# Kernel tuning notes

Hardware: AMD Instinct MI355X
Metric: run time of the kernel (lower is better)

The kernel has to match this reference:

```python
import jax, jax.numpy as jnp
import numpy as np

N, D = 8192, 256
NUM_CLASSES = 100
WEIGHT = 1.0


def setup_inputs() -> dict:
    key = jax.random.key(0)
    k1, k2 = jax.random.split(key)
    predictions = jax.random.normal(k1, (N, D), dtype=jnp.float32)
    targets = jax.random.randint(k2, (N,), 0, NUM_CLASSES, dtype=jnp.int32)
    return {"predictions": predictions, "targets": targets}


def reference(predictions, targets):
    # Pairwise squared L2 via ||a||^2 + ||b||^2 - 2 a.b  -> [N, N]
    sq = jnp.sum(predictions * predictions, axis=1)
    d2 = sq[:, None] + sq[None, :] - 2.0 * (predictions @ predictions.T)
    dist = jnp.sqrt(jnp.maximum(d2, 0.0))  # torch.dist(p=2)

    n = predictions.shape[0]
    upper = jnp.triu(jnp.ones((n, n), dtype=bool), k=1)  # i < j pairs only
    same = targets[:, None] == targets[None, :]
    mask = upper & same

    num = jnp.sum(mask).astype(dist.dtype)
    loss = jnp.sum(jnp.where(mask, dist, 0.0)) / num
    return loss * WEIGHT
```

## Files before the change

### kernel.cpp

```cpp
#include <hip/hip_runtime.h>

#define N_CLS 100
#define D_DIM 256
#define MAX_M 112
#define ROW_SH 264
#define PANEL 48

typedef short bf16x8 __attribute__((ext_vector_type(8)));
typedef float f32x4  __attribute__((ext_vector_type(4)));

__device__ __forceinline__ unsigned short f2bf(float f) {
    unsigned int b = __float_as_uint(f);
    return (unsigned short)((b + 0x7FFFu + ((b >> 16) & 1u)) >> 16);
}

__device__ __forceinline__ void stage(const float* __restrict__ pred,
        const int* bkt, int m, int cp0, int dslot, int cnt,
        short* tileS, float* sqs, int wave, int lane) {
    for (int r = wave; r < cnt; r += 8) {
        int cp = cp0 + r;
        float4 v = make_float4(0.f, 0.f, 0.f, 0.f);
        if (cp < m) {
            int g = bkt[cp];
            v = ((const float4*)(pred + (size_t)g * D_DIM))[lane];
        }
        short4 pk;
        pk.x = (short)f2bf(v.x); pk.y = (short)f2bf(v.y);
        pk.z = (short)f2bf(v.z); pk.w = (short)f2bf(v.w);
        *(short4*)&tileS[(dslot + r) * ROW_SH + lane * 4] = pk;
        float s = v.x * v.x + v.y * v.y + v.z * v.z + v.w * v.w;
        #pragma unroll
        for (int o = 32; o; o >>= 1) s += __shfl_xor(s, o, 64);
        if (lane == 0) sqs[dslot + r] = s;
    }
}

__device__ __forceinline__ float tile16(const short* tileS, const float* sqs,
        int a0, int b0, int ga0, int gb0, int m, int lane) {
    const int q = lane >> 4, l15 = lane & 15;
    const short* aP = &tileS[(a0 + l15) * ROW_SH + q * 8];
    const short* bP = &tileS[(b0 + l15) * ROW_SH + q * 8];
    f32x4 acc = {0.f, 0.f, 0.f, 0.f};
    #pragma unroll
    for (int ks = 0; ks < 8; ++ks) {
        bf16x8 af = *(const bf16x8*)(aP + ks * 32);
        bf16x8 bg = *(const bf16x8*)(bP + ks * 32);
        acc = __builtin_amdgcn_mfma_f32_16x16x32_bf16(af, bg, acc, 0, 0, 0);
    }
    float out = 0.f;
    #pragma unroll
    for (int rr = 0; rr < 4; ++rr) {
        int al = q * 4 + rr;
        int pi = ga0 + al, pj = gb0 + l15;
        float d2 = sqs[a0 + al] + sqs[b0 + l15] - 2.f * acc[rr];
        if (pj < m && pi < pj) out += sqrtf(fmaxf(d2, 0.f));
    }
    return out;
}

__global__ __launch_bounds__(512) void k_gram(const float* __restrict__ pred,
        const int* __restrict__ targets, int n, int* __restrict__ bucket_g,
        double* __restrict__ psum, double* __restrict__ pcnt, float* __restrict__ out) {
    __shared__ short tileS[MAX_M * ROW_SH];
    __shared__ float sqs[MAX_M];
    __shared__ float wsum[8];
    __shared__ int bkt_s[MAX_M];
    __shared__ int cnt_s;
    const int t = threadIdx.x, lane = t & 63, wave = t >> 6;
    const int c = blockIdx.x;
    int* bkt_g = bucket_g + (size_t)c * n;

    if (t == 0) cnt_s = 0;
    __syncthreads();
    for (int i = t; i < n; i += 512)
        if (targets[i] == c) {
            int pos = atomicAdd(&cnt_s, 1);
            if (pos < MAX_M) bkt_s[pos] = i;
            bkt_g[pos] = i;
        }
    __syncthreads();
    const int m = cnt_s;
    float accum = 0.f;

    if (m <= MAX_M) {
        const int T = (m + 15) >> 4;
        stage(pred, bkt_s, m, 0, 0, T * 16, tileS, sqs, wave, lane);
        __syncthreads();
        const int np = T * (T + 1) / 2;
        for (int idx = wave; idx < np; idx += 8) {
            int ta = 0, r = idx;
            while (r >= T - ta) { r -= T - ta; ++ta; }
            int tb = ta + r;
            accum += tile16(tileS, sqs, ta * 16, tb * 16, ta * 16, tb * 16, m, lane);
        }
    } else {
        const int P = (m + PANEL - 1) / PANEL;
        for (int pi = 0; pi < P; ++pi)
        for (int pj = pi; pj < P; ++pj) {
            __syncthreads();
            stage(pred, bkt_g, m, pi * PANEL, 0,     PANEL, tileS, sqs, wave, lane);
            stage(pred, bkt_g, m, pj * PANEL, PANEL, PANEL, tileS, sqs, wave, lane);
            __syncthreads();
            for (int idx = wave; idx < 9; idx += 8) {
                int ta = idx / 3, tb = idx % 3;
                accum += tile16(tileS, sqs, ta * 16, PANEL + tb * 16,
                                pi * PANEL + ta * 16, pj * PANEL + tb * 16, m, lane);
            }
        }
    }

    #pragma unroll
    for (int o = 32; o; o >>= 1) accum += __shfl_xor(accum, o, 64);
    if (lane == 0) wsum[wave] = accum;
    __syncthreads();
    if (t == 0) {
        double bs = 0.0;
        #pragma unroll
        for (int w = 0; w < 8; ++w) bs += (double)wsum[w];
        __hip_atomic_store(&psum[c], bs, __ATOMIC_RELAXED, __HIP_MEMORY_SCOPE_AGENT);
        __hip_atomic_store(&pcnt[c], (double)m * (double)(m - 1) * 0.5,
                           __ATOMIC_RELEASE, __HIP_MEMORY_SCOPE_AGENT);
    }

    if (c == 0) {
        double mys = 0.0, myc = 0.0;
        if (t < N_CLS) {
            unsigned long long bits;
            do {
                bits = __hip_atomic_load((const unsigned long long*)&pcnt[t],
                                         __ATOMIC_ACQUIRE, __HIP_MEMORY_SCOPE_AGENT);
            } while (bits >> 63);
            myc = __longlong_as_double((long long)bits);
            unsigned long long sb = __hip_atomic_load((const unsigned long long*)&psum[t],
                                         __ATOMIC_RELAXED, __HIP_MEMORY_SCOPE_AGENT);
            mys = __longlong_as_double((long long)sb);
        }
        __syncthreads();
        double* red_s = (double*)tileS;
        double* red_c = red_s + 128;
        if (t < 128) { red_s[t] = (t < N_CLS) ? mys : 0.0;
                       red_c[t] = (t < N_CLS) ? myc : 0.0; }
        __syncthreads();
        for (int w = 64; w; w >>= 1) {
            if (t < w) { red_s[t] += red_s[t + w]; red_c[t] += red_c[t + w]; }
            __syncthreads();
        }
        if (t == 0) out[0] = (float)(red_c[0] > 0.0 ? red_s[0] / red_c[0] : 0.0);
    }
}

extern "C" void kernel_launch(void* const* d_in, const int* in_sizes, int n_in,
                              void* d_out, int out_size, void* d_ws, size_t ws_size,
                              hipStream_t stream) {
    const float* pred  = (const float*)d_in[0];
    const int* targets = (const int*)d_in[1];
    float* out         = (float*)d_out;
    const int n = in_sizes[1];

    char* ws = (char*)d_ws;
    size_t off = 0;
    double* psum     = (double*)(ws + off); off += N_CLS * 8;
    double* pcnt     = (double*)(ws + off); off += N_CLS * 8;
    int*    bucket_g = (int*)(ws + off);

    k_gram<<<N_CLS, 512, 0, stream>>>(pred, targets, n, bucket_g, psum, pcnt, out);
}
```

Before: 74.00 us.

## Split class bucketing and bf16 packing into a separate per-row prep kernel

A new prep kernel assigns one wave per sample row. Each wave atomically appends the row to its class bucket, computes its squared norm and writes a bf16-packed copy into a per-class contiguous buffer. The gram kernel then reads the class count and copies the pre-packed tile straight into shared memory. This replaces the old scheme where each of the 100 blocks scanned all targets and gathered fp32 rows serially. The per-class counters use a poison-value offset and are reset at the end, so correctness depends on the workspace being pre-filled with that pattern; it also adds a second launch.

```diff
diff --git a/kernel.cpp b/kernel.cpp
--- a/kernel.cpp
+++ b/kernel.cpp
@@ -5,6 +5,9 @@
 #define MAX_M 112
 #define ROW_SH 264
 #define PANEL 48
+#define PACK_CAP 128
+#define CNT_STR 32
+#define POISON 0xAAAAAAAAu
 
 typedef short bf16x8 __attribute__((ext_vector_type(8)));
 typedef float f32x4  __attribute__((ext_vector_type(4)));
@@ -12,6 +15,33 @@
 __device__ __forceinline__ unsigned short f2bf(float f) {
     unsigned int b = __float_as_uint(f);
     return (unsigned short)((b + 0x7FFFu + ((b >> 16) & 1u)) >> 16);
+}
+
+__global__ __launch_bounds__(256) void k_prep(const float* __restrict__ pred,
+        const int* __restrict__ targets, int n, int* __restrict__ cnt,
+        int* __restrict__ bucket_g, float* __restrict__ sqp,
+        unsigned short* __restrict__ packed) {
+    const int wid  = (int)((blockIdx.x * 256u + threadIdx.x) >> 6);
+    const int lane = threadIdx.x & 63;
+    if (wid >= n) return;
+    const int c = targets[wid];
+    int pos = 0;
+    if (lane == 0) {
+        pos = (int)((unsigned)atomicAdd(&cnt[c * CNT_STR], 1) - POISON);
+        bucket_g[(size_t)c * n + pos] = wid;
+    }
+    pos = __shfl(pos, 0, 64);
+    const float4 v = ((const float4*)(pred + (size_t)wid * D_DIM))[lane];
+    float s = v.x * v.x + v.y * v.y + v.z * v.z + v.w * v.w;
+    #pragma unroll
+    for (int o = 32; o; o >>= 1) s += __shfl_xor(s, o, 64);
+    if (pos < PACK_CAP) {
+        short4 pk;
+        pk.x = (short)f2bf(v.x); pk.y = (short)f2bf(v.y);
+        pk.z = (short)f2bf(v.z); pk.w = (short)f2bf(v.w);
+        *(short4*)(packed + ((size_t)c * PACK_CAP + pos) * D_DIM + lane * 4) = pk;
+        if (lane == 0) sqp[c * PACK_CAP + pos] = s;
+    }
 }
 
 __device__ __forceinline__ void stage(const float* __restrict__ pred,
@@ -58,33 +88,24 @@
     return out;
 }
 
-__global__ __launch_bounds__(512) void k_gram(const float* __restrict__ pred,
-        const int* __restrict__ targets, int n, int* __restrict__ bucket_g,
+__global__ __launch_bounds__(512) void k_gram2(const float* __restrict__ pred, int n,
+        int* __restrict__ cnt, const int* __restrict__ bucket_g,
+        const float* __restrict__ sqp, const unsigned short* __restrict__ packed,
         double* __restrict__ psum, double* __restrict__ pcnt, float* __restrict__ out) {
     __shared__ short tileS[MAX_M * ROW_SH];
     __shared__ float sqs[MAX_M];
     __shared__ float wsum[8];
-    __shared__ int bkt_s[MAX_M];
-    __shared__ int cnt_s;
     const int t = threadIdx.x, lane = t & 63, wave = t >> 6;
     const int c = blockIdx.x;
-    int* bkt_g = bucket_g + (size_t)c * n;
-
-    if (t == 0) cnt_s = 0;
-    __syncthreads();
-    for (int i = t; i < n; i += 512)
-        if (targets[i] == c) {
-            int pos = atomicAdd(&cnt_s, 1);
-            if (pos < MAX_M) bkt_s[pos] = i;
-            bkt_g[pos] = i;
-        }
-    __syncthreads();
-    const int m = cnt_s;
+    const int m = (int)((unsigned)cnt[c * CNT_STR] - POISON);
     float accum = 0.f;
 
     if (m <= MAX_M) {
         const int T = (m + 15) >> 4;
-        stage(pred, bkt_s, m, 0, 0, T * 16, tileS, sqs, wave, lane);
+        const int4* srcv = (const int4*)(packed + (size_t)c * PACK_CAP * D_DIM);
+        for (int k = t; k < m * 32; k += 512)
+            *(int4*)&tileS[(k >> 5) * ROW_SH + (k & 31) * 8] = srcv[k];
+        if (t < m) sqs[t] = sqp[c * PACK_CAP + t];
         __syncthreads();
         const int np = T * (T + 1) / 2;
         for (int idx = wave; idx < np; idx += 8) {
@@ -94,6 +115,7 @@
             accum += tile16(tileS, sqs, ta * 16, tb * 16, ta * 16, tb * 16, m, lane);
         }
     } else {
+        const int* bkt_g = bucket_g + (size_t)c * n;
         const int P = (m + PANEL - 1) / PANEL;
         for (int pi = 0; pi < P; ++pi)
         for (int pj = pi; pj < P; ++pj) {
@@ -120,6 +142,7 @@
         __hip_atomic_store(&psum[c], bs, __ATOMIC_RELAXED, __HIP_MEMORY_SCOPE_AGENT);
         __hip_atomic_store(&pcnt[c], (double)m * (double)(m - 1) * 0.5,
                            __ATOMIC_RELEASE, __HIP_MEMORY_SCOPE_AGENT);
+        cnt[c * CNT_STR] = (int)POISON;
     }
 
     if (c == 0) {
@@ -159,9 +182,17 @@
 
     char* ws = (char*)d_ws;
     size_t off = 0;
-    double* psum     = (double*)(ws + off); off += N_CLS * 8;
-    double* pcnt     = (double*)(ws + off); off += N_CLS * 8;
-    int*    bucket_g = (int*)(ws + off);
+    double* psum = (double*)(ws + off); off += N_CLS * 8;
+    double* pcnt = (double*)(ws + off); off += N_CLS * 8;
+    int* cnt     = (int*)(ws + off);    off += (size_t)N_CLS * CNT_STR * 4;
+    float* sqp   = (float*)(ws + off);  off += (size_t)N_CLS * PACK_CAP * 4;
+    off = (off + 63) & ~(size_t)63;
+    unsigned short* packed = (unsigned short*)(ws + off);
+    off += (size_t)N_CLS * PACK_CAP * D_DIM * 2;
+    int* bucket_g = (int*)(ws + off);
 
-    k_gram<<<N_CLS, 512, 0, stream>>>(pred, targets, n, bucket_g, psum, pcnt, out);
+    const int prep_blocks = (n * 64 + 255) / 256;
+    k_prep<<<prep_blocks, 256, 0, stream>>>(pred, targets, n, cnt, bucket_g, sqp, packed);
+    k_gram2<<<N_CLS, 512, 0, stream>>>(pred, n, cnt, bucket_g, sqp, packed,
+                                       psum, pcnt, out);
 }
```

After: 68.72 us. 1.08x faster.

## Stage class rows via direct global-to-LDS loads and vectorize the target scan

Applied to the files above, without the earlier changes.

Rows of each class are now staged in two halves. Each half is copied straight from global memory into an fp32 LDS buffer with global_load_lds, waited on once, and then converted to bf16 together with the squared norms. This is meant to let all row loads be in flight together instead of serialising each load with its conversion. The target-bucketing scan now reads int4 vectors when n is 8192 and keeps the scalar loop as a fallback. Costs are an extra 57KB of LDS per block, and padded tile rows past m are no longer zero-filled; the existing pj<m and pi<pj masks exclude them.

```diff
diff --git a/kernel.cpp b/kernel.cpp
--- a/kernel.cpp
+++ b/kernel.cpp
@@ -5,6 +5,10 @@
 #define MAX_M 112
 #define ROW_SH 264
 #define PANEL 48
+#define HALF_R 56
+
+#define AS1 __attribute__((address_space(1)))
+#define AS3 __attribute__((address_space(3)))
 
 typedef short bf16x8 __attribute__((ext_vector_type(8)));
 typedef float f32x4  __attribute__((ext_vector_type(4)));
@@ -12,6 +16,10 @@
 __device__ __forceinline__ unsigned short f2bf(float f) {
     unsigned int b = __float_as_uint(f);
     return (unsigned short)((b + 0x7FFFu + ((b >> 16) & 1u)) >> 16);
+}
+
+__device__ __forceinline__ void gl_lds16(const void* g, void* l) {
+    __builtin_amdgcn_global_load_lds((AS1 void*)g, (AS3 void*)l, 16, 0, 0);
 }
 
 __device__ __forceinline__ void stage(const float* __restrict__ pred,
@@ -58,10 +66,11 @@
     return out;
 }
 
-__global__ __launch_bounds__(512) void k_gram(const float* __restrict__ pred,
+__global__ __launch_bounds__(512) void k_cls(const float* __restrict__ pred,
         const int* __restrict__ targets, int n, int* __restrict__ bucket_g,
         double* __restrict__ psum, double* __restrict__ pcnt, float* __restrict__ out) {
     __shared__ short tileS[MAX_M * ROW_SH];
+    __shared__ __align__(16) float fbuf[HALF_R * D_DIM];
     __shared__ float sqs[MAX_M];
     __shared__ float wsum[8];
     __shared__ int bkt_s[MAX_M];
@@ -72,20 +81,59 @@
 
     if (t == 0) cnt_s = 0;
     __syncthreads();
-    for (int i = t; i < n; i += 512)
-        if (targets[i] == c) {
-            int pos = atomicAdd(&cnt_s, 1);
-            if (pos < MAX_M) bkt_s[pos] = i;
-            bkt_g[pos] = i;
-        }
+
+    if (n == 8192) {
+        const int4* tg = (const int4*)targets;
+        int4 tv0 = tg[0 * 512 + t], tv1 = tg[1 * 512 + t],
+             tv2 = tg[2 * 512 + t], tv3 = tg[3 * 512 + t];
+        const int4 tvs[4] = {tv0, tv1, tv2, tv3};
+        #pragma unroll
+        for (int u = 0; u < 4; ++u) {
+            const int base = 4 * (u * 512 + t);
+            const int vals[4] = {tvs[u].x, tvs[u].y, tvs[u].z, tvs[u].w};
+            #pragma unroll
+            for (int e = 0; e < 4; ++e)
+                if (vals[e] == c) {
+                    int pos = atomicAdd(&cnt_s, 1);
+                    if (pos < MAX_M) bkt_s[pos] = base + e;
+                    bkt_g[pos] = base + e;
+                }
+        }
+    } else {
+        for (int i = t; i < n; i += 512)
+            if (targets[i] == c) {
+                int pos = atomicAdd(&cnt_s, 1);
+                if (pos < MAX_M) bkt_s[pos] = i;
+                bkt_g[pos] = i;
+            }
+    }
     __syncthreads();
     const int m = cnt_s;
     float accum = 0.f;
 
     if (m <= MAX_M) {
         const int T = (m + 15) >> 4;
-        stage(pred, bkt_s, m, 0, 0, T * 16, tileS, sqs, wave, lane);
-        __syncthreads();
+        #pragma unroll
+        for (int ph = 0; ph < 2; ++ph) {
+            const int r0 = ph * HALF_R;
+            const int rend = (m < r0 + HALF_R) ? m : (r0 + HALF_R);
+            for (int r = r0 + wave; r < rend; r += 8)
+                gl_lds16(pred + (size_t)bkt_s[r] * D_DIM + lane * 4,
+                         &fbuf[(r - r0) * D_DIM]);
+            asm volatile("s_waitcnt vmcnt(0)" ::: "memory");
+            for (int r = r0 + wave; r < rend; r += 8) {
+                float4 v = *(const float4*)&fbuf[(r - r0) * D_DIM + lane * 4];
+                short4 pk;
+                pk.x = (short)f2bf(v.x); pk.y = (short)f2bf(v.y);
+                pk.z = (short)f2bf(v.z); pk.w = (short)f2bf(v.w);
+                *(short4*)&tileS[r * ROW_SH + lane * 4] = pk;
+                float s = v.x * v.x + v.y * v.y + v.z * v.z + v.w * v.w;
+                #pragma unroll
+                for (int o = 32; o; o >>= 1) s += __shfl_xor(s, o, 64);
+                if (lane == 0) sqs[r] = s;
+            }
+            __syncthreads();
+        }
         const int np = T * (T + 1) / 2;
         for (int idx = wave; idx < np; idx += 8) {
             int ta = 0, r = idx;
@@ -163,5 +211,5 @@
     double* pcnt     = (double*)(ws + off); off += N_CLS * 8;
     int*    bucket_g = (int*)(ws + off);
 
-    k_gram<<<N_CLS, 512, 0, stream>>>(pred, targets, n, bucket_g, psum, pcnt, out);
-}
+    k_cls<<<N_CLS, 512, 0, stream>>>(pred, targets, n, bucket_g, psum, pcnt, out);
+}
```

Result: faster. 68.86 us (-6.9%).
